# Optimization experiments

Hardware: AMD Instinct MI355X
Metric: run time of the kernel (lower is better)

Reference implementation:

```python
import jax, jax.numpy as jnp
import numpy as np

EPS = 1e-5

def _layer_norm(x, w, b):
    mu = jnp.mean(x, axis=-1, keepdims=True)
    var = jnp.mean(jnp.square(x - mu), axis=-1, keepdims=True)
    return (x - mu) * jax.lax.rsqrt(var + EPS) * w + b

def setup_inputs() -> dict:
    B, N, C, H, CH = 1, 256, 128, 4, 32
    key = jax.random.key(0)
    ks = jax.random.split(key, 8)
    s = 0.02
    return {
        "z": jax.random.normal(ks[0], (B, N, N, C), dtype=jnp.float32),
        "pair_mask": jnp.ones((B, N, N), dtype=jnp.float32),
        "ln_w": jnp.ones((C,), dtype=jnp.float32),
        "ln_b": jnp.zeros((C,), dtype=jnp.float32),
        "Wq": jax.random.normal(ks[1], (H * CH, C), dtype=jnp.float32) * s,
        "Wk": jax.random.normal(ks[2], (H * CH, C), dtype=jnp.float32) * s,
        "Wv": jax.random.normal(ks[3], (H * CH, C), dtype=jnp.float32) * s,
        "Wb": jax.random.normal(ks[4], (H, C), dtype=jnp.float32) * s,
        "Wg": jax.random.normal(ks[5], (H * CH, C), dtype=jnp.float32) * s,
        "bg": jnp.zeros((H * CH,), dtype=jnp.float32),
        "Wo": jax.random.normal(ks[6], (C, H * CH), dtype=jnp.float32) * s,
        "bo": jnp.zeros((C,), dtype=jnp.float32),
    }

def reference(z, pair_mask, ln_w, ln_b, Wq, Wk, Wv, Wb, Wg, bg, Wo, bo):
    B, I, J, C = z.shape
    H = Wb.shape[0]
    CH = Wq.shape[0] // H
    zn = _layer_norm(z, ln_w, ln_b)                      # (B,I,J,C)
    q = (zn @ Wq.T).reshape(B, I, J, H, CH)
    k = (zn @ Wk.T).reshape(B, I, J, H, CH)
    v = (zn @ Wv.T).reshape(B, I, J, H, CH)
    bias = zn @ Wb.T                                     # (B,I,J,H) -> per-head pair bias
    g = jax.nn.sigmoid(zn @ Wg.T + bg)                   # (B,I,J,H*CH)
    scale = 1.0 / jnp.sqrt(jnp.asarray(CH, z.dtype))
    # logits[b,h,i,j,k] = q_ij . k_ik / sqrt(CH) + bias[b,h,j,k]
    logits = jnp.einsum('bijhd,bikhd->bhijk', q, k) * scale
    logits = logits + jnp.transpose(bias, (0, 3, 1, 2))[:, :, None, :, :]
    # pair mask: (B,i,j,k) outer product, True = attend
    mask2d = (pair_mask[..., :, None] * pair_mask[..., None, :]) > 0.5
    logits = jnp.where(mask2d[:, None], logits, jnp.asarray(-1e9, logits.dtype))
    probs = jax.nn.softmax(logits, axis=-1)
    o = jnp.einsum('bhijk,bikhd->bijhd', probs, v).reshape(B, I, J, H * CH)
    o = g * o
    return o @ Wo.T + bo
```

## Files before the change

kernel.cpp:

```cpp
#include <hip/hip_runtime.h>
#include <hip/hip_bf16.h>

#define ATT_SCALE 0.17677669529663687f
#define LOG2E     1.4426950408889634f

typedef __attribute__((ext_vector_type(8))) short short8v;
typedef __attribute__((ext_vector_type(4))) float f32x4;
typedef __attribute__((ext_vector_type(16))) float f32x16;

__device__ __forceinline__ short f2bf(float f) {
    unsigned u = __builtin_bit_cast(unsigned, f);
    u = u + 0x7fffu + ((u >> 16) & 1u);
    return (short)(u >> 16);
}
__device__ __forceinline__ float bf2f(short s) {
    unsigned u = ((unsigned)(unsigned short)s) << 16;
    return __builtin_bit_cast(float, u);
}
__device__ __forceinline__ unsigned pk2(float lo, float hi) {
    return (unsigned)(unsigned short)f2bf(lo) |
           ((unsigned)(unsigned short)f2bf(hi) << 16);
}
__device__ __forceinline__ float lo16f(unsigned w) {
    return __builtin_bit_cast(float, w << 16);
}
__device__ __forceinline__ float hi16f(unsigned w) {
    return __builtin_bit_cast(float, w & 0xffff0000u);
}
__device__ __forceinline__ float exp2i(float x) {
    float r;
    asm("v_exp_f32 %0, %1" : "=v"(r) : "v"(x));
    return r;
}
__device__ __forceinline__ unsigned short f2h(float f) {
    _Float16 h = (_Float16)f;
    return __builtin_bit_cast(unsigned short, h);
}
__device__ __forceinline__ float h2f(unsigned short u) {
    return (float)__builtin_bit_cast(_Float16, u);
}

__global__ __launch_bounds__(256) void k_wprep(
    const float* __restrict__ Wq, const float* __restrict__ Wk,
    const float* __restrict__ Wv, const float* __restrict__ Wg,
    const float* __restrict__ Wb, const float* __restrict__ Wo,
    unsigned short* __restrict__ wbf, unsigned short* __restrict__ wbbf,
    unsigned short* __restrict__ wohi, unsigned short* __restrict__ wolo)
{
    int idx = blockIdx.x * 256 + threadIdx.x;
    if (idx < 65536) {
        int m = idx >> 14, e = idx & 16383;
        float v;
        if (m == 0)      v = Wq[e] * (ATT_SCALE * LOG2E);
        else if (m == 1) v = Wk[e];
        else if (m == 2) v = Wv[e];
        else             v = Wg[e];
        wbf[idx] = (unsigned short)f2bf(v);
    } else if (idx < 66048) {
        int e = idx - 65536;
        wbbf[e] = (unsigned short)f2bf(Wb[e]);
    } else if (idx < 82432) {
        int e = idx - 66048;
        float w = Wo[e];
        short hv = f2bf(w);
        wohi[e] = (unsigned short)hv;
        wolo[e] = (unsigned short)f2bf(w - bf2f(hv));
    }
}

__global__ __launch_bounds__(512, 4) void k_lnproj(
    const float* __restrict__ z, const float* __restrict__ lnw,
    const float* __restrict__ lnb,
    const unsigned short* __restrict__ wbf, const unsigned short* __restrict__ wbbf,
    const float* __restrict__ bg,
    unsigned short* __restrict__ q_o, unsigned short* __restrict__ k_o,
    unsigned short* __restrict__ vt_o, unsigned short* __restrict__ g_o,
    unsigned* __restrict__ bTP)
{
    __shared__ __align__(16) short zn[128][136];
    __shared__ __align__(16) short wstg[8][32][40];

    const int tid  = threadIdx.x;
    const int lane = tid & 63;
    const int wave = tid >> 6;
    const int l15  = lane & 15;
    const int g    = lane >> 4;
    const int wr   = wave >> 2;
    const int wc   = wave & 3;
    const long p0  = (long)blockIdx.x * 128;
    const int xq   = (int)(p0 >> 8);
    const int y0   = (int)(p0 & 255);

    {
        const int r = tid >> 2, q4 = tid & 3;
        const float* zrow = z + (p0 + r) * 128 + q4 * 32;
        float4 xv[8];
        float s1 = 0.f, s2 = 0.f;
#pragma unroll
        for (int m = 0; m < 8; ++m) {
            xv[m] = *(const float4*)(zrow + m * 4);
            s1 += xv[m].x + xv[m].y + xv[m].z + xv[m].w;
            s2 += xv[m].x * xv[m].x + xv[m].y * xv[m].y +
                  xv[m].z * xv[m].z + xv[m].w * xv[m].w;
        }
        s1 += __shfl_xor(s1, 1); s2 += __shfl_xor(s2, 1);
        s1 += __shfl_xor(s1, 2); s2 += __shfl_xor(s2, 2);
        float mu  = s1 * 0.0078125f;
        float inv = rsqrtf(s2 * 0.0078125f - mu * mu + 1e-5f);
#pragma unroll
        for (int mm = 0; mm < 4; ++mm) {
            float4 a = xv[2 * mm], b = xv[2 * mm + 1];
            const float* wp = lnw + q4 * 32 + mm * 8;
            const float* bp = lnb + q4 * 32 + mm * 8;
            float4 w0 = *(const float4*)wp, w1 = *(const float4*)(wp + 4);
            float4 b0 = *(const float4*)bp, b1 = *(const float4*)(bp + 4);
            uint4 uu;
            uu.x = pk2((a.x - mu) * inv * w0.x + b0.x, (a.y - mu) * inv * w0.y + b0.y);
            uu.y = pk2((a.z - mu) * inv * w0.z + b0.z, (a.w - mu) * inv * w0.w + b0.w);
            uu.z = pk2((b.x - mu) * inv * w1.x + b1.x, (b.y - mu) * inv * w1.y + b1.y);
            uu.w = pk2((b.z - mu) * inv * w1.z + b1.z, (b.w - mu) * inv * w1.w + b1.w);
            *(uint4*)&zn[r][q4 * 32 + mm * 8] = uu;
        }
    }
    __syncthreads();

    if (wc == 0) {
        const unsigned short* wbp = wbbf + (l15 & 3) * 128;
        short8v wb[4];
#pragma unroll
        for (int ks = 0; ks < 4; ++ks)
            wb[ks] = *(const short8v*)(wbp + ks * 32 + g * 8);
        f32x4 bacc[4];
#pragma unroll
        for (int rt = 0; rt < 4; ++rt) bacc[rt] = (f32x4){0.f, 0.f, 0.f, 0.f};
#pragma unroll
        for (int ks = 0; ks < 4; ++ks)
#pragma unroll
            for (int rt = 0; rt < 4; ++rt) {
                short8v a = *(const short8v*)&zn[wr * 64 + rt * 16 + l15][ks * 32 + g * 8];
                bacc[rt] = __builtin_amdgcn_mfma_f32_16x16x32_bf16(a, wb[ks], bacc[rt], 0, 0, 0);
            }
        if (l15 < 4) {
#pragma unroll
            for (int rt = 0; rt < 4; ++rt) {
                int kb = y0 + wr * 64 + rt * 16 + g * 4;
                unsigned w0 = pk2(bacc[rt][0] * LOG2E, bacc[rt][1] * LOG2E);
                unsigned w1 = pk2(bacc[rt][2] * LOG2E, bacc[rt][3] * LOG2E);
                bTP[l15 * 32768 + (kb >> 1) * 256 + xq]       = w0;
                bTP[l15 * 32768 + ((kb >> 1) + 1) * 256 + xq] = w1;
            }
        }
    }

    for (int wsel = 0; wsel < 4; ++wsel) {
        const unsigned short* __restrict__ W = wbf + wsel * 16384;
        f32x4 acc[4][2];
#pragma unroll
        for (int rt = 0; rt < 4; ++rt) {
            acc[rt][0] = (f32x4){0.f, 0.f, 0.f, 0.f};
            acc[rt][1] = (f32x4){0.f, 0.f, 0.f, 0.f};
        }
#pragma unroll
        for (int ks = 0; ks < 4; ++ks) {
            short8v b0 = *(const short8v*)(W + (wc * 32 + l15) * 128 + ks * 32 + g * 8);
            short8v b1 = *(const short8v*)(W + (wc * 32 + 16 + l15) * 128 + ks * 32 + g * 8);
#pragma unroll
            for (int rt = 0; rt < 4; ++rt) {
                short8v a = *(const short8v*)&zn[wr * 64 + rt * 16 + l15][ks * 32 + g * 8];
                acc[rt][0] = __builtin_amdgcn_mfma_f32_16x16x32_bf16(a, b0, acc[rt][0], 0, 0, 0);
                acc[rt][1] = __builtin_amdgcn_mfma_f32_16x16x32_bf16(a, b1, acc[rt][1], 0, 0, 0);
            }
        }

        if (wsel == 3) {
#pragma unroll
            for (int ct = 0; ct < 2; ++ct) {
                float bgc = bg[wc * 32 + ct * 16 + l15];
#pragma unroll
                for (int rt = 0; rt < 4; ++rt)
#pragma unroll
                    for (int r = 0; r < 4; ++r) {
                        float val = acc[rt][ct][r] + bgc;
                        g_o[((long)wc * 65536 + p0 + wr * 64 + rt * 16 + g * 4 + r) * 32 +
                            ct * 16 + l15] = f2h(1.0f / (1.0f + __expf(-val)));
                    }
            }
        } else if (wsel == 2) {
#pragma unroll
            for (int pair = 0; pair < 2; ++pair) {
#pragma unroll
                for (int rt2 = 0; rt2 < 2; ++rt2)
#pragma unroll
                    for (int ct = 0; ct < 2; ++ct)
#pragma unroll
                        for (int r = 0; r < 4; ++r)
                            wstg[wave][ct * 16 + l15][rt2 * 16 + g * 4 + r] =
                                f2bf(acc[pair * 2 + rt2][ct][r]);
#pragma unroll
                for (int e = 0; e < 4; ++e) {
                    int idx = e * 64 + lane;
                    int d = idx >> 3, k4 = idx & 7;
                    int k4p = ((k4 & 1) << 1) | ((k4 >> 1) & 1) | (k4 & 4);
                    short4 sv = *(const short4*)&wstg[wave][d][k4 * 4];
                    *(short4*)(vt_o + (((long)wc * 256 + xq) * 32 + d) * 256 +
                               y0 + wr * 64 + pair * 32 + k4p * 4) = sv;
                }
            }
        } else {
            unsigned short* __restrict__ O = (wsel == 0) ? q_o : k_o;
#pragma unroll
            for (int pair = 0; pair < 2; ++pair) {
#pragma unroll
                for (int rt2 = 0; rt2 < 2; ++rt2)
#pragma unroll
                    for (int ct = 0; ct < 2; ++ct)
#pragma unroll
                        for (int r = 0; r < 4; ++r)
                            wstg[wave][rt2 * 16 + g * 4 + r][ct * 16 + l15] =
                                f2bf(acc[pair * 2 + rt2][ct][r]);
#pragma unroll
                for (int ps = 0; ps < 2; ++ps) {
                    int idx = ps * 64 + lane;
                    int lr = idx >> 2, ch = (idx & 3) * 8;
                    short8v vv = *(const short8v*)&wstg[wave][lr][ch];
                    *(short8v*)(O + ((long)wc * 65536 + p0 + wr * 64 + pair * 32 + lr) * 32 + ch) = vv;
                }
            }
        }
    }
}

__global__ __launch_bounds__(256, 2) void k_attn_mfma(
    const unsigned short* __restrict__ q_ws, const unsigned short* __restrict__ k_ws,
    const unsigned short* __restrict__ vt_ws, const unsigned short* __restrict__ g_ws,
    const unsigned* __restrict__ bTP, const float* __restrict__ pm,
    unsigned short* __restrict__ ob)
{
    __shared__ __align__(16) short Ksh[256][40];
    __shared__ __align__(16) short VTsh[32][264];
    __shared__ float pmsh[256];

    const int tid  = threadIdx.x;
    const int lane = tid & 63;
    const int wave = tid >> 6;
    const int l31  = lane & 31;
    const int hi   = lane >> 5;
    const int h = blockIdx.x & 3;
    const int i = blockIdx.x >> 2;
    const long hbase  = ((long)h * 65536 + (long)i * 256) * 32;
    const long vtbase = ((long)h * 256 + i) * 8192;

    pmsh[tid] = pm[i * 256 + tid];
#pragma unroll
    for (int pass = 0; pass < 4; ++pass) {
        int idx = pass * 256 + tid;
        *(short8v*)&Ksh[idx >> 2][(idx & 3) * 8] =
            *(const short8v*)(k_ws + hbase + idx * 8);
        *(short8v*)&VTsh[idx >> 5][(idx & 31) * 8] =
            *(const short8v*)(vt_ws + vtbase + idx * 8);
    }
    __syncthreads();

    bool ok4 = true;
#pragma unroll
    for (int e = 0; e < 4; ++e) ok4 = ok4 && (pmsh[lane * 4 + e] > 0.5f);
    const bool allok = __all(ok4);

    const f32x16 zero16 = {0.f,0.f,0.f,0.f,0.f,0.f,0.f,0.f,
                           0.f,0.f,0.f,0.f,0.f,0.f,0.f,0.f};

    for (int qi = 0; qi < 2; ++qi) {
        const int qb = wave * 2 + qi;
        const int ql = qb * 32 + l31;

        short8v bq0 = *(const short8v*)(q_ws + hbase + (long)ql * 32 + hi * 8);
        short8v bq1 = *(const short8v*)(q_ws + hbase + (long)ql * 32 + 16 + hi * 8);
        const bool rowok = pmsh[ql] > 0.5f;
        const unsigned* btp = bTP + h * 32768 + ql;

        const long grow = hbase + (long)ql * 32;
        ushort4 gu[4];
#pragma unroll
        for (int n = 0; n < 4; ++n)
            gu[n] = *(const ushort4*)(g_ws + grow + n * 8 + hi * 4);

        f32x16 oacc = zero16;
        float ls0 = 0.f, ls1 = 0.f;

        short8v ka0 = *(const short8v*)&Ksh[l31][hi * 8];
        short8v ka1 = *(const short8v*)&Ksh[l31][16 + hi * 8];
        short8v va0 = *(const short8v*)&VTsh[l31][hi * 8];
        short8v va1 = *(const short8v*)&VTsh[l31][16 + hi * 8];
        unsigned bb[8];
#pragma unroll
        for (int n = 0; n < 4; ++n) {
            int m = (n * 8 + hi * 4) >> 1;
            bb[2 * n]     = btp[m * 256];
            bb[2 * n + 1] = btp[(m + 1) * 256];
        }

#pragma unroll
        for (int t = 0; t < 8; ++t) {
            short8v nka0, nka1, nva0, nva1;
            unsigned nbb[8];
            if (t < 7) {
                nka0 = *(const short8v*)&Ksh[(t + 1) * 32 + l31][hi * 8];
                nka1 = *(const short8v*)&Ksh[(t + 1) * 32 + l31][16 + hi * 8];
                nva0 = *(const short8v*)&VTsh[l31][(t + 1) * 32 + hi * 8];
                nva1 = *(const short8v*)&VTsh[l31][(t + 1) * 32 + 16 + hi * 8];
#pragma unroll
                for (int n = 0; n < 4; ++n) {
                    int m = ((t + 1) * 32 + n * 8 + hi * 4) >> 1;
                    nbb[2 * n]     = btp[m * 256];
                    nbb[2 * n + 1] = btp[(m + 1) * 256];
                }
            }

            __builtin_amdgcn_s_setprio(1);
            f32x16 s = __builtin_amdgcn_mfma_f32_32x32x16_bf16(ka0, bq0, zero16, 0, 0, 0);
            s = __builtin_amdgcn_mfma_f32_32x32x16_bf16(ka1, bq1, s, 0, 0, 0);
            __builtin_amdgcn_s_setprio(0);

            uint4 w0, w1;
            if (allok) {
                float p0, p1, p2, p3;
                p0 = exp2i(s[0] + lo16f(bb[0])); p1 = exp2i(s[1] + hi16f(bb[0]));
                p2 = exp2i(s[2] + lo16f(bb[1])); p3 = exp2i(s[3] + hi16f(bb[1]));
                ls0 += (p0 + p1) + (p2 + p3);
                w0.x = pk2(p0, p1); w0.y = pk2(p2, p3);
                p0 = exp2i(s[4] + lo16f(bb[2])); p1 = exp2i(s[5] + hi16f(bb[2]));
                p2 = exp2i(s[6] + lo16f(bb[3])); p3 = exp2i(s[7] + hi16f(bb[3]));
                ls1 += (p0 + p1) + (p2 + p3);
                w0.z = pk2(p0, p1); w0.w = pk2(p2, p3);
                p0 = exp2i(s[8] + lo16f(bb[4])); p1 = exp2i(s[9] + hi16f(bb[4]));
                p2 = exp2i(s[10] + lo16f(bb[5])); p3 = exp2i(s[11] + hi16f(bb[5]));
                ls0 += (p0 + p1) + (p2 + p3);
                w1.x = pk2(p0, p1); w1.y = pk2(p2, p3);
                p0 = exp2i(s[12] + lo16f(bb[6])); p1 = exp2i(s[13] + hi16f(bb[6]));
                p2 = exp2i(s[14] + lo16f(bb[7])); p3 = exp2i(s[15] + hi16f(bb[7]));
                ls1 += (p0 + p1) + (p2 + p3);
                w1.z = pk2(p0, p1); w1.w = pk2(p2, p3);
            } else {
#pragma unroll
                for (int n = 0; n < 4; ++n) {
                    f32x4 ma = *(const f32x4*)&pmsh[t * 32 + n * 8 + hi * 4];
                    float p0 = exp2i(rowok ? s[4*n+0] + lo16f(bb[2*n])   + ((ma[0] > 0.5f) ? 0.f : -1e9f) : 0.0f);
                    float p1 = exp2i(rowok ? s[4*n+1] + hi16f(bb[2*n])   + ((ma[1] > 0.5f) ? 0.f : -1e9f) : 0.0f);
                    float p2 = exp2i(rowok ? s[4*n+2] + lo16f(bb[2*n+1]) + ((ma[2] > 0.5f) ? 0.f : -1e9f) : 0.0f);
                    float p3 = exp2i(rowok ? s[4*n+3] + hi16f(bb[2*n+1]) + ((ma[3] > 0.5f) ? 0.f : -1e9f) : 0.0f);
                    ls0 += (p0 + p1) + (p2 + p3);
                    unsigned wa = pk2(p0, p1), wb = pk2(p2, p3);
                    if (n == 0) { w0.x = wa; w0.y = wb; }
                    else if (n == 1) { w0.z = wa; w0.w = wb; }
                    else if (n == 2) { w1.x = wa; w1.y = wb; }
                    else { w1.z = wa; w1.w = wb; }
                }
            }
            short8v pb0 = *(short8v*)&w0;
            short8v pb1 = *(short8v*)&w1;

            __builtin_amdgcn_s_setprio(1);
            oacc = __builtin_amdgcn_mfma_f32_32x32x16_bf16(va0, pb0, oacc, 0, 0, 0);
            oacc = __builtin_amdgcn_mfma_f32_32x32x16_bf16(va1, pb1, oacc, 0, 0, 0);
            __builtin_amdgcn_s_setprio(0);

            if (t < 7) {
                ka0 = nka0; ka1 = nka1; va0 = nva0; va1 = nva1;
#pragma unroll
                for (int e = 0; e < 8; ++e) bb[e] = nbb[e];
            }
        }

        float lsum = ls0 + ls1;
        lsum += __shfl_xor(lsum, 32);
        const float linv = 1.0f / lsum;

        const long orow = (long)(i * 256 + ql) * 128 + h * 32;
#pragma unroll
        for (int n = 0; n < 4; ++n) {
            int dbase = n * 8 + hi * 4;
            float v0 = oacc[4 * n + 0] * linv * h2f(gu[n].x);
            float v1 = oacc[4 * n + 1] * linv * h2f(gu[n].y);
            float v2 = oacc[4 * n + 2] * linv * h2f(gu[n].z);
            float v3 = oacc[4 * n + 3] * linv * h2f(gu[n].w);
            short4 sh = {f2bf(v0), f2bf(v1), f2bf(v2), f2bf(v3)};
            *(short4*)(ob + orow + dbase) = sh;
        }
    }
}

__global__ __launch_bounds__(512, 4) void k_outproj(
    const unsigned short* __restrict__ ob,
    const unsigned short* __restrict__ wohi, const unsigned short* __restrict__ wolo,
    const float* __restrict__ bo, float* __restrict__ out)
{
    const int tid  = threadIdx.x;
    const int lane = tid & 63;
    const int wave = tid >> 6;
    const int l15  = lane & 15;
    const int g    = lane >> 4;
    const int wr   = wave >> 2;
    const int wc   = wave & 3;
    const long p0  = (long)blockIdx.x * 128;

    f32x4 acc[4][2];
#pragma unroll
    for (int rt = 0; rt < 4; ++rt) {
        acc[rt][0] = (f32x4){0.f, 0.f, 0.f, 0.f};
        acc[rt][1] = (f32x4){0.f, 0.f, 0.f, 0.f};
    }

#pragma unroll
    for (int ks = 0; ks < 4; ++ks) {
        const int wof = ks * 32 + g * 8;
        short8v bh0 = *(const short8v*)(wohi + (wc * 32 + l15) * 128 + wof);
        short8v bh1 = *(const short8v*)(wohi + (wc * 32 + 16 + l15) * 128 + wof);
        short8v bl0 = *(const short8v*)(wolo + (wc * 32 + l15) * 128 + wof);
        short8v bl1 = *(const short8v*)(wolo + (wc * 32 + 16 + l15) * 128 + wof);
#pragma unroll
        for (int rt = 0; rt < 4; ++rt) {
            long aoff = (p0 + wr * 64 + rt * 16 + l15) * 128 + ks * 32 + g * 8;
            short8v ah = *(const short8v*)(ob + aoff);
            acc[rt][0] = __builtin_amdgcn_mfma_f32_16x16x32_bf16(ah, bh0, acc[rt][0], 0, 0, 0);
            acc[rt][0] = __builtin_amdgcn_mfma_f32_16x16x32_bf16(ah, bl0, acc[rt][0], 0, 0, 0);
            acc[rt][1] = __builtin_amdgcn_mfma_f32_16x16x32_bf16(ah, bh1, acc[rt][1], 0, 0, 0);
            acc[rt][1] = __builtin_amdgcn_mfma_f32_16x16x32_bf16(ah, bl1, acc[rt][1], 0, 0, 0);
        }
    }

#pragma unroll
    for (int ct = 0; ct < 2; ++ct) {
        float bv = bo[wc * 32 + ct * 16 + l15];
#pragma unroll
        for (int rt = 0; rt < 4; ++rt)
#pragma unroll
            for (int r = 0; r < 4; ++r)
                out[(p0 + wr * 64 + rt * 16 + g * 4 + r) * 128 +
                    wc * 32 + ct * 16 + l15] = acc[rt][ct][r] + bv;
    }
}

extern "C" void kernel_launch(void* const* d_in, const int* in_sizes, int n_in,
                              void* d_out, int out_size, void* d_ws, size_t ws_size,
                              hipStream_t stream) {
    const float* z   = (const float*)d_in[0];
    const float* pm  = (const float*)d_in[1];
    const float* lnw = (const float*)d_in[2];
    const float* lnb = (const float*)d_in[3];
    const float* Wq  = (const float*)d_in[4];
    const float* Wk  = (const float*)d_in[5];
    const float* Wv  = (const float*)d_in[6];
    const float* Wb  = (const float*)d_in[7];
    const float* Wg  = (const float*)d_in[8];
    const float* bg  = (const float*)d_in[9];
    const float* Wo  = (const float*)d_in[10];
    const float* bo  = (const float*)d_in[11];
    float* out = (float*)d_out;

    unsigned short* wsS  = (unsigned short*)d_ws;
    unsigned short* wbf  = wsS;
    unsigned short* wbbf = wsS + 65536;
    unsigned short* wohi = wsS + 66048;
    unsigned short* wolo = wsS + 82432;
    unsigned* bTP        = (unsigned*)(wsS + 98816);
    unsigned short* qb   = wsS + 360960;
    unsigned short* kb   = qb + 8388608;
    unsigned short* vtb  = kb + 8388608;
    unsigned short* obw  = vtb + 8388608;
    unsigned short* ghw  = obw + 8388608;

    k_wprep<<<322, 256, 0, stream>>>(Wq, Wk, Wv, Wg, Wb, Wo, wbf, wbbf, wohi, wolo);
    k_lnproj<<<512, 512, 0, stream>>>(z, lnw, lnb, wbf, wbbf, bg, qb, kb, vtb, ghw, bTP);
    k_attn_mfma<<<1024, 256, 0, stream>>>(qb, kb, vtb, ghw, bTP, pm, obw);
    k_outproj<<<512, 512, 0, stream>>>(obw, wohi, wolo, bo, out);
}
```

Measured before the change: 91.48 us.

## Halve projection block tiles, coalesce gate stores, remap attention blocks across XCDs

New measurement: 92.68 us. No clear change (+1.3%).

```diff
diff --git a/kernel.cpp b/kernel.cpp
--- a/kernel.cpp
+++ b/kernel.cpp
@@ -68,7 +68,7 @@
     }
 }
 
-__global__ __launch_bounds__(512, 4) void k_lnproj(
+__global__ __launch_bounds__(256, 4) void k_lnproj(
     const float* __restrict__ z, const float* __restrict__ lnw,
     const float* __restrict__ lnb,
     const unsigned short* __restrict__ wbf, const unsigned short* __restrict__ wbbf,
@@ -77,17 +77,16 @@
     unsigned short* __restrict__ vt_o, unsigned short* __restrict__ g_o,
     unsigned* __restrict__ bTP)
 {
-    __shared__ __align__(16) short zn[128][136];
-    __shared__ __align__(16) short wstg[8][32][40];
+    __shared__ __align__(16) short zn[64][136];
+    __shared__ __align__(16) short wstg[4][32][40];
 
     const int tid  = threadIdx.x;
     const int lane = tid & 63;
     const int wave = tid >> 6;
     const int l15  = lane & 15;
     const int g    = lane >> 4;
-    const int wr   = wave >> 2;
-    const int wc   = wave & 3;
-    const long p0  = (long)blockIdx.x * 128;
+    const int wc   = wave;
+    const long p0  = (long)blockIdx.x * 64;
     const int xq   = (int)(p0 >> 8);
     const int y0   = (int)(p0 & 255);
 
@@ -137,13 +136,13 @@
         for (int ks = 0; ks < 4; ++ks)
 #pragma unroll
             for (int rt = 0; rt < 4; ++rt) {
-                short8v a = *(const short8v*)&zn[wr * 64 + rt * 16 + l15][ks * 32 + g * 8];
+                short8v a = *(const short8v*)&zn[rt * 16 + l15][ks * 32 + g * 8];
                 bacc[rt] = __builtin_amdgcn_mfma_f32_16x16x32_bf16(a, wb[ks], bacc[rt], 0, 0, 0);
             }
         if (l15 < 4) {
 #pragma unroll
             for (int rt = 0; rt < 4; ++rt) {
-                int kb = y0 + wr * 64 + rt * 16 + g * 4;
+                int kb = y0 + rt * 16 + g * 4;
                 unsigned w0 = pk2(bacc[rt][0] * LOG2E, bacc[rt][1] * LOG2E);
                 unsigned w1 = pk2(bacc[rt][2] * LOG2E, bacc[rt][3] * LOG2E);
                 bTP[l15 * 32768 + (kb >> 1) * 256 + xq]       = w0;
@@ -166,7 +165,7 @@
             short8v b1 = *(const short8v*)(W + (wc * 32 + 16 + l15) * 128 + ks * 32 + g * 8);
 #pragma unroll
             for (int rt = 0; rt < 4; ++rt) {
-                short8v a = *(const short8v*)&zn[wr * 64 + rt * 16 + l15][ks * 32 + g * 8];
+                short8v a = *(const short8v*)&zn[rt * 16 + l15][ks * 32 + g * 8];
                 acc[rt][0] = __builtin_amdgcn_mfma_f32_16x16x32_bf16(a, b0, acc[rt][0], 0, 0, 0);
                 acc[rt][1] = __builtin_amdgcn_mfma_f32_16x16x32_bf16(a, b1, acc[rt][1], 0, 0, 0);
             }
@@ -174,16 +173,26 @@
 
         if (wsel == 3) {
 #pragma unroll
-            for (int ct = 0; ct < 2; ++ct) {
-                float bgc = bg[wc * 32 + ct * 16 + l15];
-#pragma unroll
-                for (int rt = 0; rt < 4; ++rt)
-#pragma unroll
-                    for (int r = 0; r < 4; ++r) {
-                        float val = acc[rt][ct][r] + bgc;
-                        g_o[((long)wc * 65536 + p0 + wr * 64 + rt * 16 + g * 4 + r) * 32 +
-                            ct * 16 + l15] = f2h(1.0f / (1.0f + __expf(-val)));
+            for (int pair = 0; pair < 2; ++pair) {
+#pragma unroll
+                for (int rt2 = 0; rt2 < 2; ++rt2)
+#pragma unroll
+                    for (int ct = 0; ct < 2; ++ct) {
+                        float bgc = bg[wc * 32 + ct * 16 + l15];
+#pragma unroll
+                        for (int r = 0; r < 4; ++r) {
+                            float val = acc[pair * 2 + rt2][ct][r] + bgc;
+                            wstg[wave][rt2 * 16 + g * 4 + r][ct * 16 + l15] =
+                                (short)f2h(1.0f / (1.0f + __expf(-val)));
+                        }
                     }
+#pragma unroll
+                for (int ps = 0; ps < 2; ++ps) {
+                    int idx = ps * 64 + lane;
+                    int lr = idx >> 2, ch = (idx & 3) * 8;
+                    short8v vv = *(const short8v*)&wstg[wave][lr][ch];
+                    *(short8v*)(g_o + ((long)wc * 65536 + p0 + pair * 32 + lr) * 32 + ch) = vv;
+                }
             }
         } else if (wsel == 2) {
 #pragma unroll
@@ -191,11 +200,12 @@
 #pragma unroll
                 for (int rt2 = 0; rt2 < 2; ++rt2)
 #pragma unroll
-                    for (int ct = 0; ct < 2; ++ct)
-#pragma unroll
-                        for (int r = 0; r < 4; ++r)
-                            wstg[wave][ct * 16 + l15][rt2 * 16 + g * 4 + r] =
-                                f2bf(acc[pair * 2 + rt2][ct][r]);
+                    for (int ct = 0; ct < 2; ++ct) {
+                        uint2 pw;
+                        pw.x = pk2(acc[pair * 2 + rt2][ct][0], acc[pair * 2 + rt2][ct][1]);
+                        pw.y = pk2(acc[pair * 2 + rt2][ct][2], acc[pair * 2 + rt2][ct][3]);
+                        *(uint2*)&wstg[wave][ct * 16 + l15][rt2 * 16 + g * 4] = pw;
+                    }
 #pragma unroll
                 for (int e = 0; e < 4; ++e) {
                     int idx = e * 64 + lane;
@@ -203,7 +213,7 @@
                     int k4p = ((k4 & 1) << 1) | ((k4 >> 1) & 1) | (k4 & 4);
                     short4 sv = *(const short4*)&wstg[wave][d][k4 * 4];
                     *(short4*)(vt_o + (((long)wc * 256 + xq) * 32 + d) * 256 +
-                               y0 + wr * 64 + pair * 32 + k4p * 4) = sv;
+                               y0 + pair * 32 + k4p * 4) = sv;
                 }
             }
         } else {
@@ -223,7 +233,7 @@
                     int idx = ps * 64 + lane;
                     int lr = idx >> 2, ch = (idx & 3) * 8;
                     short8v vv = *(const short8v*)&wstg[wave][lr][ch];
-                    *(short8v*)(O + ((long)wc * 65536 + p0 + wr * 64 + pair * 32 + lr) * 32 + ch) = vv;
+                    *(short8v*)(O + ((long)wc * 65536 + p0 + pair * 32 + lr) * 32 + ch) = vv;
                 }
             }
         }
@@ -245,8 +255,10 @@
     const int wave = tid >> 6;
     const int l31  = lane & 31;
     const int hi   = lane >> 5;
-    const int h = blockIdx.x & 3;
-    const int i = blockIdx.x >> 2;
+    const int bid = blockIdx.x;
+    const int xcd = bid & 7, jj = bid >> 3;
+    const int h = xcd >> 1;
+    const int i = ((xcd & 1) << 7) | jj;
     const long hbase  = ((long)h * 65536 + (long)i * 256) * 32;
     const long vtbase = ((long)h * 256 + i) * 8192;
 
@@ -389,7 +401,7 @@
     }
 }
 
-__global__ __launch_bounds__(512, 4) void k_outproj(
+__global__ __launch_bounds__(256, 4) void k_outproj(
     const unsigned short* __restrict__ ob,
     const unsigned short* __restrict__ wohi, const unsigned short* __restrict__ wolo,
     const float* __restrict__ bo, float* __restrict__ out)
@@ -399,9 +411,8 @@
     const int wave = tid >> 6;
     const int l15  = lane & 15;
     const int g    = lane >> 4;
-    const int wr   = wave >> 2;
-    const int wc   = wave & 3;
-    const long p0  = (long)blockIdx.x * 128;
+    const int wc   = wave;
+    const long p0  = (long)blockIdx.x * 64;
 
     f32x4 acc[4][2];
 #pragma unroll
@@ -419,7 +430,7 @@
         short8v bl1 = *(const short8v*)(wolo + (wc * 32 + 16 + l15) * 128 + wof);
 #pragma unroll
         for (int rt = 0; rt < 4; ++rt) {
-            long aoff = (p0 + wr * 64 + rt * 16 + l15) * 128 + ks * 32 + g * 8;
+            long aoff = (p0 + rt * 16 + l15) * 128 + ks * 32 + g * 8;
             short8v ah = *(const short8v*)(ob + aoff);
             acc[rt][0] = __builtin_amdgcn_mfma_f32_16x16x32_bf16(ah, bh0, acc[rt][0], 0, 0, 0);
             acc[rt][0] = __builtin_amdgcn_mfma_f32_16x16x32_bf16(ah, bl0, acc[rt][0], 0, 0, 0);
@@ -435,7 +446,7 @@
         for (int rt = 0; rt < 4; ++rt)
 #pragma unroll
             for (int r = 0; r < 4; ++r)
-                out[(p0 + wr * 64 + rt * 16 + g * 4 + r) * 128 +
+                out[(p0 + rt * 16 + g * 4 + r) * 128 +
                     wc * 32 + ct * 16 + l15] = acc[rt][ct][r] + bv;
     }
 }
@@ -470,7 +481,7 @@
     unsigned short* ghw  = obw + 8388608;
 
     k_wprep<<<322, 256, 0, stream>>>(Wq, Wk, Wv, Wg, Wb, Wo, wbf, wbbf, wohi, wolo);
-    k_lnproj<<<512, 512, 0, stream>>>(z, lnw, lnb, wbf, wbbf, bg, qb, kb, vtb, ghw, bTP);
+    k_lnproj<<<1024, 256, 0, stream>>>(z, lnw, lnb, wbf, wbbf, bg, qb, kb, vtb, ghw, bTP);
     k_attn_mfma<<<1024, 256, 0, stream>>>(qb, kb, vtb, ghw, bTP, pm, obw);
-    k_outproj<<<512, 512, 0, stream>>>(obw, wohi, wolo, bo, out);
-}
+    k_outproj<<<1024, 256, 0, stream>>>(obw, wohi, wolo, bo, out);
+}
```
